# Optimization experiments

Hardware: AMD Instinct MI355X
Metric: run time of the kernel (lower is better)

The kernel has to match this reference:

```python
import jax, jax.numpy as jnp
import numpy as np


def setup_inputs() -> dict:
    key = jax.random.key(0)
    images = jax.random.uniform(key, (64, 384, 384, 3), dtype=jnp.float32)
    return {"images": images, "k": 5}


def reference(images, k):
    # cv2.dilate with a k x k kernel of ones == per-channel max filter with SAME padding.
    # Applied over the whole batch in one fused reduce_window (window only over H, W).
    out = jax.lax.reduce_window(
        images,
        -jnp.inf,
        jax.lax.max,
        window_dimensions=(1, k, k, 1),
        window_strides=(1, 1, 1, 1),
        padding="SAME",
    )
    # cv_to_tf appends a trailing singleton dim before tf.stack -> (B, H, W, C, 1)
    return out[..., None]
```

## Files before the change

kernel.cpp:

```cpp
#include <hip/hip_runtime.h>
#include <hip/hip_bf16.h>


#define Bn 64
#define H 384
#define ROWF 1152
#define ROWBYTES (ROWF * 4)
#define WF4 288
#define RB 12
#define NLOAD (RB + 4)
#define GROUPS 8
#define STRIPS 5
#define SOUT 60
#define NEGINF (-3.402823466e+38f)

__device__ __forceinline__ float4 max4(float4 a, float4 b) {
  return make_float4(fmaxf(a.x, b.x), fmaxf(a.y, b.y),
                     fmaxf(a.z, b.z), fmaxf(a.w, b.w));
}
__device__ __forceinline__ float4 shflup4(float4 v, int d) {
  return make_float4(__shfl_up(v.x, d), __shfl_up(v.y, d),
                     __shfl_up(v.z, d), __shfl_up(v.w, d));
}
__device__ __forceinline__ float4 shfldn4(float4 v, int d) {
  return make_float4(__shfl_down(v.x, d), __shfl_down(v.y, d),
                     __shfl_down(v.z, d), __shfl_down(v.w, d));
}

__global__ __launch_bounds__(256) void dilate5_kernel(
    const float* __restrict__ in, float* __restrict__ out) {
  const int wv = threadIdx.x >> 6;
  const int lane = threadIdx.x & 63;
  int t = blockIdx.x;
  const int strip = t % STRIPS; t /= STRIPS;
  const int grp = t % GROUPS;   t /= GROUPS;
  const int b = t;

  const int row0 = (grp * 4 + wv) * RB;
  const int col = strip * SOUT - 2 + lane;
  const bool cvalid = (col >= 0) && (col < WF4);
  const int ccl = col < 0 ? 0 : (col > WF4 - 1 ? WF4 - 1 : col);
  const size_t coff = (size_t)ccl * 16;
  const bool willstore = (lane >= 2) && (lane < 62) && (col < WF4);

  const float4 ninf = make_float4(NEGINF, NEGINF, NEGINF, NEGINF);
  const char* __restrict__ imgb = (const char*)in + (size_t)b * H * ROWBYTES;
  char* __restrict__ outb = (char*)out + (size_t)b * H * ROWBYTES;

  float4 raw[NLOAD];
#pragma unroll
  for (int j = 0; j < NLOAD; ++j) {
    int gh = row0 - 2 + j;
    int ghc = gh < 0 ? 0 : (gh > H - 1 ? H - 1 : gh);
    raw[j] = *reinterpret_cast<const float4*>(imgb + (size_t)ghc * ROWBYTES + coff);
  }

  auto hcomb = [&](int gh, float4 Cv) -> float4 {
    if (!cvalid) Cv = ninf;
    float4 A = shflup4(Cv, 2);
    float4 Bv = shflup4(Cv, 1);
    float4 D = shfldn4(Cv, 1);
    float4 E = shfldn4(Cv, 2);
    float4 h;
    h.x = fmaxf(fmaxf(fmaxf(A.z, Bv.y), fmaxf(Cv.x, Cv.w)), D.z);
    h.y = fmaxf(fmaxf(fmaxf(A.w, Bv.z), fmaxf(Cv.y, D.x)), D.w);
    h.z = fmaxf(fmaxf(fmaxf(Bv.x, Bv.w), fmaxf(Cv.z, D.y)), E.x);
    h.w = fmaxf(fmaxf(fmaxf(Bv.y, Cv.x), fmaxf(Cv.w, D.z)), E.y);
    if (gh < 0 || gh >= H) h = ninf;
    return h;
  };

  float4 r0 = hcomb(row0 - 2, raw[0]);
  float4 r1 = hcomb(row0 - 1, raw[1]);
  float4 r2 = hcomb(row0,     raw[2]);
  float4 r3 = hcomb(row0 + 1, raw[3]);

#pragma unroll
  for (int i = 0; i < RB; ++i) {
    const int o = row0 + i;
    float4 r4 = hcomb(o + 2, raw[i + 4]);
    float4 v = max4(max4(max4(r0, r1), max4(r2, r3)), r4);
    if (willstore)
      *reinterpret_cast<float4*>(outb + (size_t)o * ROWBYTES + coff) = v;
    r0 = r1; r1 = r2; r2 = r3; r3 = r4;
  }
}

extern "C" void kernel_launch(void* const* d_in, const int* in_sizes, int n_in,
                              void* d_out, int out_size, void* d_ws, size_t ws_size,
                              hipStream_t stream) {
  const float* images = (const float*)d_in[0];
  float* out = (float*)d_out;
  const int nblocks = Bn * GROUPS * STRIPS;
  dilate5_kernel<<<nblocks, 256, 0, stream>>>(images, out);
}
```

Measured before the change: 202.8 us.

## Reorder separable max to vertical-first, add nontemporal stores and block remap

```diff
diff --git a/kernel.cpp b/kernel.cpp
--- a/kernel.cpp
+++ b/kernel.cpp
@@ -1,5 +1,4 @@
 #include <hip/hip_runtime.h>
-#include <hip/hip_bf16.h>
 
 
 #define Bn 64
@@ -12,7 +11,10 @@
 #define GROUPS 8
 #define STRIPS 5
 #define SOUT 60
+#define NBLK (Bn * GROUPS * STRIPS)
 #define NEGINF (-3.402823466e+38f)
+
+typedef float f32x4 __attribute__((ext_vector_type(4)));
 
 __device__ __forceinline__ float4 max4(float4 a, float4 b) {
   return make_float4(fmaxf(a.x, b.x), fmaxf(a.y, b.y),
@@ -27,11 +29,13 @@
                      __shfl_down(v.z, d), __shfl_down(v.w, d));
 }
 
-__global__ __launch_bounds__(256) void dilate5_kernel(
+__global__ __launch_bounds__(256, 4) void dilate5_kernel(
     const float* __restrict__ in, float* __restrict__ out) {
   const int wv = threadIdx.x >> 6;
   const int lane = threadIdx.x & 63;
-  int t = blockIdx.x;
+
+  const int orig = blockIdx.x;
+  int t = (orig & 7) * (NBLK / 8) + (orig >> 3);
   const int strip = t % STRIPS; t /= STRIPS;
   const int grp = t % GROUPS;   t /= GROUPS;
   const int b = t;
@@ -55,34 +59,31 @@
     raw[j] = *reinterpret_cast<const float4*>(imgb + (size_t)ghc * ROWBYTES + coff);
   }
 
-  auto hcomb = [&](int gh, float4 Cv) -> float4 {
-    if (!cvalid) Cv = ninf;
-    float4 A = shflup4(Cv, 2);
-    float4 Bv = shflup4(Cv, 1);
-    float4 D = shfldn4(Cv, 1);
-    float4 E = shfldn4(Cv, 2);
-    float4 h;
-    h.x = fmaxf(fmaxf(fmaxf(A.z, Bv.y), fmaxf(Cv.x, Cv.w)), D.z);
-    h.y = fmaxf(fmaxf(fmaxf(A.w, Bv.z), fmaxf(Cv.y, D.x)), D.w);
-    h.z = fmaxf(fmaxf(fmaxf(Bv.x, Bv.w), fmaxf(Cv.z, D.y)), E.x);
-    h.w = fmaxf(fmaxf(fmaxf(Bv.y, Cv.x), fmaxf(Cv.w, D.z)), E.y);
-    if (gh < 0 || gh >= H) h = ninf;
-    return h;
-  };
-
-  float4 r0 = hcomb(row0 - 2, raw[0]);
-  float4 r1 = hcomb(row0 - 1, raw[1]);
-  float4 r2 = hcomb(row0,     raw[2]);
-  float4 r3 = hcomb(row0 + 1, raw[3]);
+  if (row0 == 0)      { raw[0] = ninf; raw[1] = ninf; }
+  if (row0 == H - RB) { raw[NLOAD - 2] = ninf; raw[NLOAD - 1] = ninf; }
 
 #pragma unroll
   for (int i = 0; i < RB; ++i) {
     const int o = row0 + i;
-    float4 r4 = hcomb(o + 2, raw[i + 4]);
-    float4 v = max4(max4(max4(r0, r1), max4(r2, r3)), r4);
-    if (willstore)
-      *reinterpret_cast<float4*>(outb + (size_t)o * ROWBYTES + coff) = v;
-    r0 = r1; r1 = r2; r2 = r3; r3 = r4;
+    float4 v = max4(max4(max4(raw[i], raw[i + 1]), max4(raw[i + 2], raw[i + 3])),
+                    raw[i + 4]);
+    if (!cvalid) v = ninf;
+
+    float4 A = shflup4(v, 2);
+    float4 Bv = shflup4(v, 1);
+    float4 D = shfldn4(v, 1);
+    float4 E = shfldn4(v, 2);
+    float4 h;
+    h.x = fmaxf(fmaxf(fmaxf(A.z, Bv.y), fmaxf(v.x, v.w)), D.z);
+    h.y = fmaxf(fmaxf(fmaxf(A.w, Bv.z), fmaxf(v.y, D.x)), D.w);
+    h.z = fmaxf(fmaxf(fmaxf(Bv.x, Bv.w), fmaxf(v.z, D.y)), E.x);
+    h.w = fmaxf(fmaxf(fmaxf(Bv.y, v.x), fmaxf(v.w, D.z)), E.y);
+
+    if (willstore) {
+      f32x4 hv; hv.x = h.x; hv.y = h.y; hv.z = h.z; hv.w = h.w;
+      __builtin_nontemporal_store(
+          hv, reinterpret_cast<f32x4*>(outb + (size_t)o * ROWBYTES + coff));
+    }
   }
 }
 
@@ -91,6 +92,5 @@
                               hipStream_t stream) {
   const float* images = (const float*)d_in[0];
   float* out = (float*)d_out;
-  const int nblocks = Bn * GROUPS * STRIPS;
-  dilate5_kernel<<<nblocks, 256, 0, stream>>>(images, out);
+  dilate5_kernel<<<NBLK, 256, 0, stream>>>(images, out);
 }
```

After: 204.2 us. No clear change (+0.7%).
